# Kernel optimization log

Measured on AMD Instinct MI355X. Metric: run time of the kernel, lower is better.

The kernel has to match this reference:

```python
import jax, jax.numpy as jnp
import numpy as np

B, S, D = 4, 4096, 1024
C = 8.0

def setup_inputs() -> dict:
    key = jax.random.key(0)
    k_x, k_wa, k_wx, k_ba, k_bx, k_lam = jax.random.split(key, 6)
    x = jax.random.normal(k_x, (B, S, D), dtype=jnp.float32)
    std = 1.0 / np.sqrt(D)
    Wa = jax.random.normal(k_wa, (D, D), dtype=jnp.float32) * std
    Wx = jax.random.normal(k_wx, (D, D), dtype=jnp.float32) * std
    ba = jax.random.normal(k_ba, (D,), dtype=jnp.float32) * 0.02
    bx = jax.random.normal(k_bx, (D,), dtype=jnp.float32) * 0.02
    # Lambda init: u ~ U(0.9, 0.999); Lambda = -log(u^{-1/c} - 1)
    u = jax.random.uniform(k_lam, (D,), dtype=jnp.float32, minval=0.9, maxval=0.999)
    Lam = -jnp.log(jnp.power(u, -1.0 / C) - 1.0)
    return {"x": x, "Wa": Wa, "Wx": Wx, "ba": ba, "bx": bx, "Lam": Lam}

def reference(x, Wa, Wx, ba, bx, Lam):
    # gates for all timesteps at once (two GEMMs)
    rt = jax.nn.sigmoid(jnp.einsum('bsd,hd->bsh', x, Wa) + ba)   # recurrence gate
    it = jax.nn.sigmoid(jnp.einsum('bsd,hd->bsh', x, Wx) + bx)   # input gate
    log_a = -C * jax.nn.softplus(-Lam) * rt                      # (B,S,D)
    a = jnp.exp(log_a)
    b = jnp.sqrt(1.0 - a * a) * (it * x)                         # (B,S,D)
    # sequential diagonal linear recurrence h_t = a_t * h_{t-1} + b_t
    def step(h, ab):
        a_t, b_t = ab
        h = a_t * h + b_t
        return h, h
    h0 = jnp.zeros((x.shape[0], x.shape[2]), dtype=x.dtype)
    _, y = jax.lax.scan(step, h0, (jnp.swapaxes(a, 0, 1), jnp.swapaxes(b, 0, 1)))
    return jnp.swapaxes(y, 0, 1)  # (B,S,D)
```

## Files before the change

### kernel.cpp

```cpp
#include <hip/hip_runtime.h>
#include <hip/hip_bf16.h>
#include <math.h>

#define BDIM 4
#define SLEN 4096
#define DDIM 1024
#define MROWS (BDIM*SLEN)
#define KDIM DDIM
#define NCHUNK 64
#define CLEN (SLEN/NCHUNK)
#define NCH (BDIM*DDIM)
#define NKT (KDIM/32)
#define LDSBUF 16384
#define ALLROWS (MROWS + 2*DDIM)

typedef __bf16 bf16;
typedef __bf16 bf16x8 __attribute__((ext_vector_type(8)));
typedef float f32x16 __attribute__((ext_vector_type(16)));

__device__ __forceinline__ void gload_lds16(const void* g, void* l) {
  __builtin_amdgcn_global_load_lds(
      (const __attribute__((address_space(1))) unsigned int*)g,
      (__attribute__((address_space(3))) unsigned int*)l, 16, 0, 0);
}

__global__ void cast_all_kernel(const float* __restrict__ x, const float* __restrict__ Wa,
                                const float* __restrict__ Wx, bf16* __restrict__ out) {
  const int gid  = blockIdx.x * 256 + threadIdx.x;
  const int tile = gid >> 7, local = gid & 127;
  const int j = local & 3, r = local >> 2;
  const int T = tile >> 5, KT = tile & 31;
  const int m = T*32 + r;
  const float* src;
  int row;
  if (m < MROWS)              { src = x;  row = m; }
  else if (m < MROWS + DDIM)  { src = Wa; row = m - MROWS; }
  else                        { src = Wx; row = m - MROWS - DDIM; }
  const float4* p = (const float4*)(src + (size_t)row * KDIM + KT*32 + j*8);
  float4 v0 = p[0], v1 = p[1];
  bf16x8 o;
  o[0] = (bf16)v0.x; o[1] = (bf16)v0.y; o[2] = (bf16)v0.z; o[3] = (bf16)v0.w;
  o[4] = (bf16)v1.x; o[5] = (bf16)v1.y; o[6] = (bf16)v1.z; o[7] = (bf16)v1.w;
  ((bf16x8*)out)[(size_t)tile * 128 + j*32 + r] = o;
}

__global__ void klam_kernel(const float* __restrict__ Lam, float* __restrict__ klam) {
  int h = blockIdx.x * blockDim.x + threadIdx.x;
  if (h < DDIM) klam[h] = -8.0f * 1.4426950408889634f * log1pf(__expf(-Lam[h]));
}

__global__ __launch_bounds__(256, 3) void gemm_gates_kernel(
    const bf16* __restrict__ xb, const bf16* __restrict__ wab, const bf16* __restrict__ wxb,
    const float* __restrict__ ba, const float* __restrict__ bx,
    const float* __restrict__ klam, bf16* __restrict__ La, bf16* __restrict__ Bp,
    float* __restrict__ sAo, float* __restrict__ sBo)
{
  __shared__ char smem[3*LDSBUF];

  const int tid  = threadIdx.x;
  const int wave = tid >> 6, lane = tid & 63;
  const int wm = wave >> 1, wn = wave & 1;

  const int orig  = blockIdx.x;
  const int newid = (orig & 7) * 256 + (orig >> 3);
  const int m0 = (newid >> 4) * 128;
  const int h0 = (newid & 15) * 64;

  f32x16 accA0 = (f32x16)0.0f, accA1 = (f32x16)0.0f;
  f32x16 accX0 = (f32x16)0.0f, accX1 = (f32x16)0.0f;

  const int Tb = m0 >> 5;
  const int Ht = h0 >> 5;
  const bf16* xsrc0 = xb  + (size_t)(Tb + (tid >> 7)) * 32768 + (tid & 127) * 8;
  const bf16* xsrc1 = xsrc0 + 2 * 32768;
  const bf16* wsrcA = wab + (size_t)(Ht + (tid >> 7)) * 32768 + (tid & 127) * 8;
  const bf16* wsrcX = wxb + (size_t)(Ht + (tid >> 7)) * 32768 + (tid & 127) * 8;

  auto STAGE = [&](int KT, char* nb) {
    gload_lds16(xsrc0 + KT*1024, nb + tid*16);
    gload_lds16(xsrc1 + KT*1024, nb + 4096  + tid*16);
    gload_lds16(wsrcA + KT*1024, nb + 8192  + tid*16);
    gload_lds16(wsrcX + KT*1024, nb + 12288 + tid*16);
  };

  const int awoff  = wm*4096  + lane*16;
  const int bwoffA = 8192  + wn*2048 + lane*16;
  const int bwoffX = 12288 + wn*2048 + lane*16;

  char* b0 = smem;
  char* b1 = smem + LDSBUF;
  char* b2 = smem + 2*LDSBUF;

  STAGE(0, b0);
  STAGE(1, b1);
  asm volatile("s_waitcnt vmcnt(4)" ::: "memory");
  __builtin_amdgcn_s_barrier();

  char *pc = b0, *pn = b1, *ps = b2;
  for (int kt = 0; kt < NKT; ++kt) {
    bf16x8 a00 = *(const bf16x8*)(pc + awoff);
    bf16x8 a01 = *(const bf16x8*)(pc + awoff + 1024);
    bf16x8 a10 = *(const bf16x8*)(pc + awoff + 2048);
    bf16x8 a11 = *(const bf16x8*)(pc + awoff + 3072);
    bf16x8 ba0 = *(const bf16x8*)(pc + bwoffA);
    bf16x8 ba1 = *(const bf16x8*)(pc + bwoffA + 1024);
    bf16x8 bx0 = *(const bf16x8*)(pc + bwoffX);
    bf16x8 bx1 = *(const bf16x8*)(pc + bwoffX + 1024);
    __builtin_amdgcn_sched_barrier(0);

    if (kt + 2 < NKT) STAGE(kt + 2, ps);

    __builtin_amdgcn_s_barrier();
    asm volatile("s_waitcnt lgkmcnt(0)" ::: "memory");
    __builtin_amdgcn_sched_barrier(0);

    __builtin_amdgcn_s_setprio(1);
    accA0 = __builtin_amdgcn_mfma_f32_32x32x16_bf16(a00, ba0, accA0, 0, 0, 0);
    accA1 = __builtin_amdgcn_mfma_f32_32x32x16_bf16(a10, ba0, accA1, 0, 0, 0);
    accX0 = __builtin_amdgcn_mfma_f32_32x32x16_bf16(a00, bx0, accX0, 0, 0, 0);
    accX1 = __builtin_amdgcn_mfma_f32_32x32x16_bf16(a10, bx0, accX1, 0, 0, 0);
    accA0 = __builtin_amdgcn_mfma_f32_32x32x16_bf16(a01, ba1, accA0, 0, 0, 0);
    accA1 = __builtin_amdgcn_mfma_f32_32x32x16_bf16(a11, ba1, accA1, 0, 0, 0);
    accX0 = __builtin_amdgcn_mfma_f32_32x32x16_bf16(a01, bx1, accX0, 0, 0, 0);
    accX1 = __builtin_amdgcn_mfma_f32_32x32x16_bf16(a11, bx1, accX1, 0, 0, 0);
    __builtin_amdgcn_s_setprio(0);

    if (kt + 2 < NKT)      { asm volatile("s_waitcnt vmcnt(4)" ::: "memory"); }
    else if (kt + 1 < NKT) { asm volatile("s_waitcnt vmcnt(0)" ::: "memory"); }
    if (kt + 1 < NKT) __builtin_amdgcn_s_barrier();

    char* tmp = pc; pc = pn; pn = ps; ps = tmp;
  }

  const int colh = h0 + wn*32 + (lane & 31);
  const int hi   = lane >> 5;
  const float bah = ba[colh], bxh = bx[colh], kl = klam[colh];
  const size_t xh = (size_t)(colh >> 5) * 1024 + ((colh >> 3) & 3) * 256 + (colh & 7);

  float P[2][4], S[2][4];
  #pragma unroll
  for (int mt = 0; mt < 2; ++mt) {
    const int mbase = m0 + wm*64 + mt*32;
    const size_t xtb = (size_t)(mbase >> 5) * 32768 + xh;
    const f32x16 aA = mt ? accA1 : accA0;
    const f32x16 aX = mt ? accX1 : accX0;
    #pragma unroll
    for (int g = 0; g < 4; ++g) {
      float Pg = 1.0f, Sg = 0.0f;
      #pragma unroll
      for (int jj = 0; jj < 4; ++jj) {
        const int q   = g*4 + jj;
        const int row = jj + 8*g + 4*hi;
        const int m   = mbase + row;
        const float ga = aA[q] + bah;
        const float gx = aX[q] + bxh;
        const float rt = 1.0f / (1.0f + __expf(-ga));
        const float it = 1.0f / (1.0f + __expf(-gx));
        const float la = kl * rt;
        const float a  = exp2f(la);
        const float xv = (float)xb[xtb + (size_t)row * 8];
        const float bb = sqrtf(fmaxf(1.0f - a*a, 0.0f)) * (it * xv);
        La[(size_t)m * DDIM + colh] = (bf16)la;
        Bp[(size_t)m * DDIM + colh] = (bf16)bb;
        Sg = fmaf(a, Sg, bb);
        Pg *= a;
      }
      P[mt][g] = Pg; S[mt][g] = Sg;
    }
  }

  float Pc = 1.0f, Sc = 0.0f;
  #pragma unroll
  for (int mt = 0; mt < 2; ++mt) {
    #pragma unroll
    for (int g = 0; g < 4; ++g) {
      const float pm = P[mt][g], sm = S[mt][g];
      const float pp = __shfl_xor(pm, 32);
      const float sp = __shfl_xor(sm, 32);
      const float p0 = hi ? pp : pm, s0 = hi ? sp : sm;
      const float p1 = hi ? pm : pp, s1 = hi ? sm : sp;
      Sc = fmaf(p0, Sc, s0); Pc *= p0;
      Sc = fmaf(p1, Sc, s1); Pc *= p1;
    }
  }
  if (hi == 0) {
    const int mb0  = m0 + wm*64;
    const int bidx = mb0 >> 12;
    const int c    = (mb0 & (SLEN-1)) >> 6;
    sAo[(size_t)c * NCH + bidx*1024 + colh] = Pc;
    sBo[(size_t)c * NCH + bidx*1024 + colh] = Sc;
  }
}

__global__ void scan2_kernel(const float* __restrict__ sA, const float* __restrict__ sB,
                             float* __restrict__ Hin) {
  const int ch = blockIdx.x * 256 + threadIdx.x;
  float h = 0.0f;
  for (int c = 0; c < NCHUNK; ++c) {
    Hin[c * NCH + ch] = h;
    h = fmaf(sA[c * NCH + ch], h, sB[c * NCH + ch]);
  }
}

__global__ void scan3_kernel(const bf16* __restrict__ La, const bf16* __restrict__ Bp,
                             const float* __restrict__ Hin, float* __restrict__ y) {
  const int ch = blockIdx.x * 256 + threadIdx.x;
  const int c  = blockIdx.y;
  const int b  = ch >> 10, d = ch & 1023;
  size_t idx = ((size_t)b * SLEN + (size_t)c * CLEN) * DDIM + d;
  float h = Hin[c * NCH + ch];
  #pragma unroll 4
  for (int s = 0; s < CLEN; ++s) {
    const float a = exp2f((float)La[idx]);
    h = fmaf(a, h, (float)Bp[idx]);
    y[idx] = h;
    idx += DDIM;
  }
}

extern "C" void kernel_launch(void* const* d_in, const int* in_sizes, int n_in,
                              void* d_out, int out_size, void* d_ws, size_t ws_size,
                              hipStream_t stream) {
  const float* x   = (const float*)d_in[0];
  const float* Wa  = (const float*)d_in[1];
  const float* Wx  = (const float*)d_in[2];
  const float* ba  = (const float*)d_in[3];
  const float* bx  = (const float*)d_in[4];
  const float* Lam = (const float*)d_in[5];
  float* y = (float*)d_out;

  if (ws_size < 108007424ULL) return;
  char* ws = (char*)d_ws;
  bf16*  xb   = (bf16*)(ws);
  bf16*  wab  = (bf16*)(ws + 33554432);
  bf16*  wxb  = (bf16*)(ws + 35651584);
  bf16*  Bp   = (bf16*)(ws + 37748736);
  bf16*  La   = (bf16*)(ws + 71303168);
  float* klam = (float*)(ws + 104857600);
  float* sA   = (float*)(ws + 104861696);
  float* sB   = (float*)(ws + 105910272);
  float* Hin  = (float*)(ws + 106958848);

  cast_all_kernel<<<(ALLROWS/32)*(KDIM/32)*128/256, 256, 0, stream>>>(x, Wa, Wx, xb);
  klam_kernel<<<DDIM/256, 256, 0, stream>>>(Lam, klam);

  gemm_gates_kernel<<<2048, 256, 0, stream>>>(xb, wab, wxb, ba, bx, klam,
                                              La, Bp, sA, sB);

  scan2_kernel<<<NCH/256, 256, 0, stream>>>(sA, sB, Hin);
  dim3 sgrid(NCH/256, NCHUNK);
  scan3_kernel<<<sgrid, 256, 0, stream>>>(La, Bp, Hin, y);
}
```

Baseline: 140.9 us.

## Enlarge gate GEMM block tile to 256x64 with eight waves

Doubles the M extent of each GEMM block from 128 to 256 rows. It uses 512 threads (8 waves), so each staged weight tile is shared by twice as many x rows, and the grid halves. The staging is rewritten to three LDS loads per thread into a larger 24KB buffer, with the vmcnt waits adjusted to match. The launch bound now asks for 4 blocks of 512 threads, which may squeeze the register budget and force spills. The larger LDS footprint also limits how many blocks fit per CU.

```diff
diff --git a/kernel.cpp b/kernel.cpp
--- a/kernel.cpp
+++ b/kernel.cpp
@@ -11,7 +11,7 @@
 #define CLEN (SLEN/NCHUNK)
 #define NCH (BDIM*DDIM)
 #define NKT (KDIM/32)
-#define LDSBUF 16384
+#define LDSBUF 24576
 #define ALLROWS (MROWS + 2*DDIM)
 
 typedef __bf16 bf16;
@@ -49,7 +49,7 @@
   if (h < DDIM) klam[h] = -8.0f * 1.4426950408889634f * log1pf(__expf(-Lam[h]));
 }
 
-__global__ __launch_bounds__(256, 3) void gemm_gates_kernel(
+__global__ __launch_bounds__(512, 4) void gemm_gates_kernel(
     const bf16* __restrict__ xb, const bf16* __restrict__ wab, const bf16* __restrict__ wxb,
     const float* __restrict__ ba, const float* __restrict__ bx,
     const float* __restrict__ klam, bf16* __restrict__ La, bf16* __restrict__ Bp,
@@ -62,8 +62,8 @@
   const int wm = wave >> 1, wn = wave & 1;
 
   const int orig  = blockIdx.x;
-  const int newid = (orig & 7) * 256 + (orig >> 3);
-  const int m0 = (newid >> 4) * 128;
+  const int newid = (orig & 7) * 128 + (orig >> 3);
+  const int m0 = (newid >> 4) * 256;
   const int h0 = (newid & 15) * 64;
 
   f32x16 accA0 = (f32x16)0.0f, accA1 = (f32x16)0.0f;
@@ -71,21 +71,23 @@
 
   const int Tb = m0 >> 5;
   const int Ht = h0 >> 5;
-  const bf16* xsrc0 = xb  + (size_t)(Tb + (tid >> 7)) * 32768 + (tid & 127) * 8;
-  const bf16* xsrc1 = xsrc0 + 2 * 32768;
-  const bf16* wsrcA = wab + (size_t)(Ht + (tid >> 7)) * 32768 + (tid & 127) * 8;
-  const bf16* wsrcX = wxb + (size_t)(Ht + (tid >> 7)) * 32768 + (tid & 127) * 8;
+  const int tt = tid >> 7;
+  const int gg = (tid & 127) * 8;
+  const bf16* aS0 = xb + (size_t)(Tb + tt)     * 32768 + gg;
+  const bf16* aS1 = xb + (size_t)(Tb + 4 + tt) * 32768 + gg;
+  const bf16* wS = (tid < 256)
+      ? wab + (size_t)(Ht + tt)     * 32768 + gg
+      : wxb + (size_t)(Ht + tt - 2) * 32768 + gg;
 
   auto STAGE = [&](int KT, char* nb) {
-    gload_lds16(xsrc0 + KT*1024, nb + tid*16);
-    gload_lds16(xsrc1 + KT*1024, nb + 4096  + tid*16);
-    gload_lds16(wsrcA + KT*1024, nb + 8192  + tid*16);
-    gload_lds16(wsrcX + KT*1024, nb + 12288 + tid*16);
+    gload_lds16(aS0 + KT*1024, nb + tid*16);
+    gload_lds16(aS1 + KT*1024, nb + 8192 + tid*16);
+    gload_lds16(wS  + KT*1024, nb + 16384 + tid*16);
   };
 
-  const int awoff  = wm*4096  + lane*16;
-  const int bwoffA = 8192  + wn*2048 + lane*16;
-  const int bwoffX = 12288 + wn*2048 + lane*16;
+  const int aOff = wm*4096  + lane*16;
+  const int bOa  = 16384 + wn*2048 + lane*16;
+  const int bOx  = 20480 + wn*2048 + lane*16;
 
   char* b0 = smem;
   char* b1 = smem + LDSBUF;
@@ -93,19 +95,19 @@
 
   STAGE(0, b0);
   STAGE(1, b1);
-  asm volatile("s_waitcnt vmcnt(4)" ::: "memory");
+  asm volatile("s_waitcnt vmcnt(3)" ::: "memory");
   __builtin_amdgcn_s_barrier();
 
   char *pc = b0, *pn = b1, *ps = b2;
   for (int kt = 0; kt < NKT; ++kt) {
-    bf16x8 a00 = *(const bf16x8*)(pc + awoff);
-    bf16x8 a01 = *(const bf16x8*)(pc + awoff + 1024);
-    bf16x8 a10 = *(const bf16x8*)(pc + awoff + 2048);
-    bf16x8 a11 = *(const bf16x8*)(pc + awoff + 3072);
-    bf16x8 ba0 = *(const bf16x8*)(pc + bwoffA);
-    bf16x8 ba1 = *(const bf16x8*)(pc + bwoffA + 1024);
-    bf16x8 bx0 = *(const bf16x8*)(pc + bwoffX);
-    bf16x8 bx1 = *(const bf16x8*)(pc + bwoffX + 1024);
+    bf16x8 a00 = *(const bf16x8*)(pc + aOff);
+    bf16x8 a01 = *(const bf16x8*)(pc + aOff + 1024);
+    bf16x8 a10 = *(const bf16x8*)(pc + aOff + 2048);
+    bf16x8 a11 = *(const bf16x8*)(pc + aOff + 3072);
+    bf16x8 ba0 = *(const bf16x8*)(pc + bOa);
+    bf16x8 ba1 = *(const bf16x8*)(pc + bOa + 1024);
+    bf16x8 bx0 = *(const bf16x8*)(pc + bOx);
+    bf16x8 bx1 = *(const bf16x8*)(pc + bOx + 1024);
     __builtin_amdgcn_sched_barrier(0);
 
     if (kt + 2 < NKT) STAGE(kt + 2, ps);
@@ -125,7 +127,7 @@
     accX1 = __builtin_amdgcn_mfma_f32_32x32x16_bf16(a11, bx1, accX1, 0, 0, 0);
     __builtin_amdgcn_s_setprio(0);
 
-    if (kt + 2 < NKT)      { asm volatile("s_waitcnt vmcnt(4)" ::: "memory"); }
+    if (kt + 2 < NKT)      { asm volatile("s_waitcnt vmcnt(3)" ::: "memory"); }
     else if (kt + 1 < NKT) { asm volatile("s_waitcnt vmcnt(0)" ::: "memory"); }
     if (kt + 1 < NKT) __builtin_amdgcn_s_barrier();
 
@@ -244,7 +246,7 @@
   cast_all_kernel<<<(ALLROWS/32)*(KDIM/32)*128/256, 256, 0, stream>>>(x, Wa, Wx, xb);
   klam_kernel<<<DDIM/256, 256, 0, stream>>>(Lam, klam);
 
-  gemm_gates_kernel<<<2048, 256, 0, stream>>>(xb, wab, wxb, ba, bx, klam,
+  gemm_gates_kernel<<<1024, 512, 0, stream>>>(xb, wab, wxb, ba, bx, klam,
                                               La, Bp, sA, sB);
 
   scan2_kernel<<<NCH/256, 256, 0, stream>>>(sA, sB, Hin);
```

Result: no change. 140.8 us (-0.1%).

## Load GEMM B-operand fragments directly into registers instead of staging through LDS

Applied to the files above, without the earlier changes.

The weight tiles for both gate GEMMs are now read straight from global memory into per-wave register fragments, prefetched two k-steps ahead with double-buffered register sets. Only the x tile is staged through LDS, which halves the LDS footprint and the LDS reads per iteration. The intent is to cut LDS traffic and allow more resident blocks. In exchange it adds register pressure and redundant global and L2 traffic, since each wave pair loads the same weight fragments, and the hand-set vmcnt counts must match the new load mix exactly.

```diff
diff --git a/kernel.cpp b/kernel.cpp
--- a/kernel.cpp
+++ b/kernel.cpp
@@ -11,7 +11,7 @@
 #define CLEN (SLEN/NCHUNK)
 #define NCH (BDIM*DDIM)
 #define NKT (KDIM/32)
-#define LDSBUF 16384
+#define ABUF 8192
 #define ALLROWS (MROWS + 2*DDIM)
 
 typedef __bf16 bf16;
@@ -55,7 +55,7 @@
     const float* __restrict__ klam, bf16* __restrict__ La, bf16* __restrict__ Bp,
     float* __restrict__ sAo, float* __restrict__ sBo)
 {
-  __shared__ char smem[3*LDSBUF];
+  __shared__ char smem[3*ABUF];
 
   const int tid  = threadIdx.x;
   const int wave = tid >> 6, lane = tid & 63;
@@ -71,66 +71,75 @@
 
   const int Tb = m0 >> 5;
   const int Ht = h0 >> 5;
-  const bf16* xsrc0 = xb  + (size_t)(Tb + (tid >> 7)) * 32768 + (tid & 127) * 8;
-  const bf16* xsrc1 = xsrc0 + 2 * 32768;
-  const bf16* wsrcA = wab + (size_t)(Ht + (tid >> 7)) * 32768 + (tid & 127) * 8;
-  const bf16* wsrcX = wxb + (size_t)(Ht + (tid >> 7)) * 32768 + (tid & 127) * 8;
-
-  auto STAGE = [&](int KT, char* nb) {
-    gload_lds16(xsrc0 + KT*1024, nb + tid*16);
-    gload_lds16(xsrc1 + KT*1024, nb + 4096  + tid*16);
-    gload_lds16(wsrcA + KT*1024, nb + 8192  + tid*16);
-    gload_lds16(wsrcX + KT*1024, nb + 12288 + tid*16);
+  const bf16* aS0 = xb + (size_t)(Tb + (tid >> 7))     * 32768 + (tid & 127) * 8;
+  const bf16* aS1 = xb + (size_t)(Tb + 2 + (tid >> 7)) * 32768 + (tid & 127) * 8;
+
+  auto STAGE_A = [&](int KT, char* nb) {
+    gload_lds16(aS0 + KT*1024, nb + tid*16);
+    gload_lds16(aS1 + KT*1024, nb + 4096 + tid*16);
   };
 
-  const int awoff  = wm*4096  + lane*16;
-  const int bwoffA = 8192  + wn*2048 + lane*16;
-  const int bwoffX = 12288 + wn*2048 + lane*16;
+  const bf16* baBase = wab + (size_t)(Ht + wn) * 32768 + (size_t)lane * 8;
+  const bf16* bxBase = wxb + (size_t)(Ht + wn) * 32768 + (size_t)lane * 8;
+
+#define LOADB(KT, BA0, BA1, BX0, BX1) do {                        \
+    const bf16* _pa = baBase + (size_t)(KT) * 1024;               \
+    const bf16* _px = bxBase + (size_t)(KT) * 1024;               \
+    BA0 = *(const bf16x8*)(_pa);  BA1 = *(const bf16x8*)(_pa + 512); \
+    BX0 = *(const bf16x8*)(_px);  BX1 = *(const bf16x8*)(_px + 512); \
+  } while (0)
+
+  const int aOff = wm*4096 + lane*16;
 
   char* b0 = smem;
-  char* b1 = smem + LDSBUF;
-  char* b2 = smem + 2*LDSBUF;
-
-  STAGE(0, b0);
-  STAGE(1, b1);
-  asm volatile("s_waitcnt vmcnt(4)" ::: "memory");
+  char* b1 = smem + ABUF;
+  char* b2 = smem + 2*ABUF;
+
+  bf16x8 ba0_0, ba1_0, bx0_0, bx1_0;
+  bf16x8 ba0_1, ba1_1, bx0_1, bx1_1;
+
+  STAGE_A(0, b0);
+  STAGE_A(1, b1);
+  LOADB(0, ba0_0, ba1_0, bx0_0, bx1_0);
+  LOADB(1, ba0_1, ba1_1, bx0_1, bx1_1);
+  asm volatile("s_waitcnt vmcnt(10)" ::: "memory");
   __builtin_amdgcn_s_barrier();
 
   char *pc = b0, *pn = b1, *ps = b2;
-  for (int kt = 0; kt < NKT; ++kt) {
-    bf16x8 a00 = *(const bf16x8*)(pc + awoff);
-    bf16x8 a01 = *(const bf16x8*)(pc + awoff + 1024);
-    bf16x8 a10 = *(const bf16x8*)(pc + awoff + 2048);
-    bf16x8 a11 = *(const bf16x8*)(pc + awoff + 3072);
-    bf16x8 ba0 = *(const bf16x8*)(pc + bwoffA);
-    bf16x8 ba1 = *(const bf16x8*)(pc + bwoffA + 1024);
-    bf16x8 bx0 = *(const bf16x8*)(pc + bwoffX);
-    bf16x8 bx1 = *(const bf16x8*)(pc + bwoffX + 1024);
-    __builtin_amdgcn_sched_barrier(0);
-
-    if (kt + 2 < NKT) STAGE(kt + 2, ps);
-
-    __builtin_amdgcn_s_barrier();
-    asm volatile("s_waitcnt lgkmcnt(0)" ::: "memory");
-    __builtin_amdgcn_sched_barrier(0);
-
-    __builtin_amdgcn_s_setprio(1);
-    accA0 = __builtin_amdgcn_mfma_f32_32x32x16_bf16(a00, ba0, accA0, 0, 0, 0);
-    accA1 = __builtin_amdgcn_mfma_f32_32x32x16_bf16(a10, ba0, accA1, 0, 0, 0);
-    accX0 = __builtin_amdgcn_mfma_f32_32x32x16_bf16(a00, bx0, accX0, 0, 0, 0);
-    accX1 = __builtin_amdgcn_mfma_f32_32x32x16_bf16(a10, bx0, accX1, 0, 0, 0);
-    accA0 = __builtin_amdgcn_mfma_f32_32x32x16_bf16(a01, ba1, accA0, 0, 0, 0);
-    accA1 = __builtin_amdgcn_mfma_f32_32x32x16_bf16(a11, ba1, accA1, 0, 0, 0);
-    accX0 = __builtin_amdgcn_mfma_f32_32x32x16_bf16(a01, bx1, accX0, 0, 0, 0);
-    accX1 = __builtin_amdgcn_mfma_f32_32x32x16_bf16(a11, bx1, accX1, 0, 0, 0);
-    __builtin_amdgcn_s_setprio(0);
-
-    if (kt + 2 < NKT)      { asm volatile("s_waitcnt vmcnt(4)" ::: "memory"); }
-    else if (kt + 1 < NKT) { asm volatile("s_waitcnt vmcnt(0)" ::: "memory"); }
-    if (kt + 1 < NKT) __builtin_amdgcn_s_barrier();
-
-    char* tmp = pc; pc = pn; pn = ps; ps = tmp;
-  }
+
+#define BODY(KT, BA0, BA1, BX0, BX1) do {                                      \
+    bf16x8 a00 = *(const bf16x8*)(pc + aOff);                                  \
+    bf16x8 a01 = *(const bf16x8*)(pc + aOff + 1024);                           \
+    bf16x8 a10 = *(const bf16x8*)(pc + aOff + 2048);                           \
+    bf16x8 a11 = *(const bf16x8*)(pc + aOff + 3072);                           \
+    __builtin_amdgcn_sched_barrier(0);                                         \
+    if ((KT) + 2 < NKT) STAGE_A((KT) + 2, ps);                                 \
+    __builtin_amdgcn_s_barrier();                      \
+    asm volatile("s_waitcnt lgkmcnt(0)" ::: "memory");                         \
+    __builtin_amdgcn_sched_barrier(0);                           \
+    __builtin_amdgcn_s_setprio(1);                                             \
+    accA0 = __builtin_amdgcn_mfma_f32_32x32x16_bf16(a00, BA0, accA0, 0, 0, 0); \
+    accA1 = __builtin_amdgcn_mfma_f32_32x32x16_bf16(a10, BA0, accA1, 0, 0, 0); \
+    accX0 = __builtin_amdgcn_mfma_f32_32x32x16_bf16(a00, BX0, accX0, 0, 0, 0); \
+    accX1 = __builtin_amdgcn_mfma_f32_32x32x16_bf16(a10, BX0, accX1, 0, 0, 0); \
+    accA0 = __builtin_amdgcn_mfma_f32_32x32x16_bf16(a01, BA1, accA0, 0, 0, 0); \
+    accA1 = __builtin_amdgcn_mfma_f32_32x32x16_bf16(a11, BA1, accA1, 0, 0, 0); \
+    accX0 = __builtin_amdgcn_mfma_f32_32x32x16_bf16(a01, BX1, accX0, 0, 0, 0); \
+    accX1 = __builtin_amdgcn_mfma_f32_32x32x16_bf16(a11, BX1, accX1, 0, 0, 0); \
+    __builtin_amdgcn_s_setprio(0);                                             \
+    if ((KT) + 2 < NKT) LOADB((KT) + 2, BA0, BA1, BX0, BX1);                   \
+    if ((KT) + 2 < NKT)      { asm volatile("s_waitcnt vmcnt(10)" ::: "memory"); } \
+    else if ((KT) + 1 < NKT) { asm volatile("s_waitcnt vmcnt(4)"  ::: "memory"); } \
+    if ((KT) + 1 < NKT) __builtin_amdgcn_s_barrier();                          \
+    char* _t = pc; pc = pn; pn = ps; ps = _t;                                  \
+  } while (0)
+
+  for (int kt = 0; kt < NKT; kt += 2) {
+    BODY(kt,     ba0_0, ba1_0, bx0_0, bx1_0);
+    BODY(kt + 1, ba0_1, ba1_1, bx0_1, bx1_1);
+  }
+#undef BODY
+#undef LOADB
 
   const int colh = h0 + wn*32 + (lane & 31);
   const int hi   = lane >> 5;
```

Measured after the change: 146.5 us. 4.0% more time.
